# Optimization experiments

Hardware: AMD Instinct MI355X
Metric: run time of the kernel (lower is better)

## Reference

```python
import jax, jax.numpy as jnp
import numpy as np

B, I, H = 256, 512, 512


def _lin_init(k, out_dim, in_dim):
    bound = 1.0 / np.sqrt(in_dim)
    kw, kb = jax.random.split(k)
    W = jax.random.uniform(kw, (out_dim, in_dim), minval=-bound, maxval=bound, dtype=jnp.float32)
    b = jax.random.uniform(kb, (out_dim,), minval=-bound, maxval=bound, dtype=jnp.float32)
    return W, b


def setup_inputs() -> dict:
    key = jax.random.key(0)
    ks = jax.random.split(key, 16)
    inp = {}
    inp['inputs'] = jax.random.normal(ks[0], (B, I), dtype=jnp.float32)
    inp['h0'] = jax.random.normal(ks[1], (B, H), dtype=jnp.float32) * 0.1
    inp['c0'] = jax.random.normal(ks[2], (B, H), dtype=jnp.float32) * 0.1
    inp['hebb'] = jax.random.uniform(ks[3], (B, H, H), minval=-0.01, maxval=0.01, dtype=jnp.float32)
    # plastic recurrent weights: w = 0.02*rand - 0.01, alpha = 1e-4*rand
    inp['w'] = 0.02 * jax.random.uniform(ks[4], (H, H), dtype=jnp.float32) - 0.01
    inp['alpha'] = 1e-4 * jax.random.uniform(ks[5], (1, 1, H), dtype=jnp.float32)
    inp['Wxf'], inp['bxf'] = _lin_init(ks[6], H, I)
    inp['Whf'], inp['bhf'] = _lin_init(ks[7], H, H)
    inp['Wxi'], inp['bxi'] = _lin_init(ks[8], H, I)
    inp['Whi'], inp['bhi'] = _lin_init(ks[9], H, H)
    inp['Wxo'], inp['bxo'] = _lin_init(ks[10], H, I)
    inp['Who'], inp['bho'] = _lin_init(ks[11], H, H)
    inp['Wxc'], inp['bxc'] = _lin_init(ks[12], H, I)
    inp['Wmod'], inp['bmod'] = _lin_init(ks[13], 1, H)   # h2mod: H -> 1
    inp['Wfan'], inp['bfan'] = _lin_init(ks[14], H, 1)   # modfanout: 1 -> H
    return inp


def reference(inputs, h0, c0, hebb, w, alpha,
              Wxf, bxf, Whf, bhf, Wxi, bxi, Whi, bhi,
              Wxo, bxo, Who, bho, Wxc, bxc, Wmod, bmod, Wfan, bfan):
    # gates (torch Linear: y = x @ W.T + b)
    fgt = jax.nn.sigmoid(inputs @ Wxf.T + bxf + h0 @ Whf.T + bhf)
    ipt = jax.nn.sigmoid(inputs @ Wxi.T + bxi + h0 @ Whi.T + bhi)
    opt = jax.nn.sigmoid(inputs @ Wxo.T + bxo + h0 @ Who.T + bho)
    # plastic recurrent path: h0 @ (w + alpha * hebb), per-sample fast weights
    h2c = jnp.einsum('bh,bhk->bk', h0, w + alpha * hebb)
    inputstocell = jnp.tanh(inputs @ Wxc.T + bxc + h2c)
    cell = fgt * c0 + ipt * inputstocell
    hactiv = opt * jnp.tanh(cell)
    # Hebbian outer-product trace update with neuromodulated learning rate
    deltahebb = jnp.einsum('bh,bk->bhk', h0, inputstocell)  # [B,H,H]
    myeta = jnp.tanh(hactiv @ Wmod.T + bmod)                # [B,1]
    myeta = myeta * Wfan[:, 0][None, :] + bfan              # modfanout(1->H): [B,H]
    hebb_new = jnp.clip(hebb + myeta[:, None, :] * deltahebb, -2.0, 2.0)
    return hactiv, cell, hebb_new
```

## Files before the change

### kernel.cpp

```cpp
#include <hip/hip_runtime.h>
#include <math.h>

#define B_ 256
#define I_ 512
#define H_ 512
#define BH (B_*H_)
#define NCH 8
#define HCH (H_/NCH)

typedef float f4v __attribute__((ext_vector_type(4)));


#define TK 16
#define LDT2 34
#define TILE_F (TK*LDT2)
#define NGEMM 512

__global__ __launch_bounds__(256) void k_dot_gates(
    const float* __restrict__ hebb, const float* __restrict__ h0,
    const float* __restrict__ inputs,
    const float* __restrict__ Wxf, const float* __restrict__ bxf,
    const float* __restrict__ Whf, const float* __restrict__ bhf,
    const float* __restrict__ Wxi, const float* __restrict__ bxi,
    const float* __restrict__ Whi, const float* __restrict__ bhi,
    const float* __restrict__ Wxo, const float* __restrict__ bxo,
    const float* __restrict__ Who, const float* __restrict__ bho,
    const float* __restrict__ Wxc, const float* __restrict__ bxc,
    const float* __restrict__ w,
    float* __restrict__ pre, float* __restrict__ part) {

    __shared__ float smem[4 * TILE_F];
    int bid = blockIdx.x;
    int tid = threadIdx.x;

    if (bid < NGEMM) {
        int n0  = (bid >> 3) * 32;
        int m0  = (bid & 7) * 32;
        int g   = n0 >> 9;
        int ko0 = n0 & 511;

        const float* Wx; const float* Wh;
        if (g == 0)      { Wx = Wxf; Wh = Whf; }
        else if (g == 1) { Wx = Wxi; Wh = Whi; }
        else if (g == 2) { Wx = Wxo; Wh = Who; }
        else             { Wx = Wxc; Wh = w;   }

        int tx = tid & 15, ty = tid >> 4;
        int lk = tid & 15, lm = tid >> 4;
        int kk2 = tid >> 4, ln0 = tid & 15;

        float acc[2][2] = {{0.f, 0.f}, {0.f, 0.f}};
        float ar[2], br[2];

        auto LOAD = [&](int t) {
            int k0 = t * TK;
            const float* Ab = (k0 < 512) ? inputs : h0;
            int kbase = k0 & 511;
            #pragma unroll
            for (int p = 0; p < 2; ++p)
                ar[p] = Ab[(size_t)(m0 + lm + 16 * p) * 512 + kbase + lk];
            if (g == 3 && k0 >= 512) {
                #pragma unroll
                for (int p = 0; p < 2; ++p)
                    br[p] = w[(size_t)(kbase + kk2) * 512 + ko0 + ln0 + 16 * p];
            } else {
                const float* Wm = (k0 < 512) ? Wx : Wh;
                #pragma unroll
                for (int p = 0; p < 2; ++p)
                    br[p] = Wm[(size_t)(ko0 + lm + 16 * p) * 512 + kbase + lk];
            }
        };
        auto STORE = [&](int t, int pbuf) {
            float* Asb = smem + pbuf * 2 * TILE_F;
            float* Bsb = Asb + TILE_F;
            int k0 = t * TK;
            #pragma unroll
            for (int p = 0; p < 2; ++p)
                Asb[lk * LDT2 + lm + 16 * p] = ar[p];
            if (g == 3 && k0 >= 512) {
                #pragma unroll
                for (int p = 0; p < 2; ++p)
                    Bsb[kk2 * LDT2 + ln0 + 16 * p] = br[p];
            } else {
                #pragma unroll
                for (int p = 0; p < 2; ++p)
                    Bsb[lk * LDT2 + lm + 16 * p] = br[p];
            }
        };

        LOAD(0);
        STORE(0, 0);
        for (int t = 0; t < 64; ++t) {
            __syncthreads();
            if (t < 63) LOAD(t + 1);
            int pb = t & 1;
            const float* Asb = smem + pb * 2 * TILE_F;
            const float* Bsb = Asb + TILE_F;
            #pragma unroll
            for (int kk = 0; kk < TK; ++kk) {
                float2 a2 = *(const float2*)&Asb[kk * LDT2 + ty * 2];
                float2 b2 = *(const float2*)&Bsb[kk * LDT2 + tx * 2];
                acc[0][0] += a2.x * b2.x; acc[0][1] += a2.x * b2.y;
                acc[1][0] += a2.y * b2.x; acc[1][1] += a2.y * b2.y;
            }
            if (t < 63) STORE(t + 1, pb ^ 1);
        }

        #pragma unroll
        for (int j = 0; j < 2; ++j) {
            int ko = ko0 + tx * 2 + j;
            float bias;
            if (g == 0)      bias = bxf[ko] + bhf[ko];
            else if (g == 1) bias = bxi[ko] + bhi[ko];
            else if (g == 2) bias = bxo[ko] + bho[ko];
            else             bias = bxc[ko];
            #pragma unroll
            for (int i = 0; i < 2; ++i) {
                int bnum = m0 + ty * 2 + i;
                pre[(size_t)g * BH + (size_t)bnum * H_ + ko] = acc[i][j] + bias;
            }
        }
    } else {
        int hbid = bid - NGEMM;
        int b  = hbid >> 3;
        int ch = hbid & 7;

        float*  h0s = smem;
        float4* red = (float4*)(smem + 64);

        if (tid < HCH) h0s[tid] = h0[b * H_ + ch * HCH + tid];
        __syncthreads();

        const float4* hbp = (const float4*)(hebb + ((size_t)b * H_ + (size_t)ch * HCH) * H_);
        int tk = tid & 127;
        int th = tid >> 7;
        float4 acc = make_float4(0.f, 0.f, 0.f, 0.f);
        #pragma unroll 8
        for (int r = 0; r < 32; ++r) {
            int hh = th * 32 + r;
            float s = h0s[hh];
            float4 vv = hbp[(size_t)hh * 128 + tk];
            acc.x += s * vv.x; acc.y += s * vv.y;
            acc.z += s * vv.z; acc.w += s * vv.w;
        }
        red[tid] = acc;
        __syncthreads();
        if (tid < 128) {
            float4 a = red[tid], c = red[tid + 128];
            float4 o = make_float4(a.x + c.x, a.y + c.y, a.z + c.z, a.w + c.w);
            ((float4*)(part + ((size_t)ch * B_ + b) * H_))[tid] = o;
        }
    }
}

__global__ __launch_bounds__(256) void k_finalize(
    const float* __restrict__ pre, const float* __restrict__ part,
    const float* __restrict__ c0, const float* __restrict__ alpha,
    const float* __restrict__ Wmod, const float* __restrict__ bmod,
    const float* __restrict__ Wfan, const float* __restrict__ bfan,
    float* __restrict__ out, float* __restrict__ v) {

    int b = blockIdx.x;
    int t = threadIdx.x;

    float c2r[2];
    float local = 0.f;
    #pragma unroll
    for (int s = 0; s < 2; ++s) {
        int k = t + s * 256;
        float dot = 0.f;
        #pragma unroll
        for (int c = 0; c < NCH; ++c) dot += part[((size_t)c * B_ + b) * H_ + k];
        float pf = pre[0 * BH + (size_t)b * H_ + k];
        float pi = pre[1 * BH + (size_t)b * H_ + k];
        float po = pre[2 * BH + (size_t)b * H_ + k];
        float pc = pre[3 * BH + (size_t)b * H_ + k];
        float c2 = tanhf(pc + alpha[k] * dot);
        float fg = 1.f / (1.f + expf(-pf));
        float ig = 1.f / (1.f + expf(-pi));
        float og = 1.f / (1.f + expf(-po));
        float cell = fg * c0[(size_t)b * H_ + k] + ig * c2;
        float ha = og * tanhf(cell);
        out[(size_t)b * H_ + k] = ha;
        out[BH + (size_t)b * H_ + k] = cell;
        c2r[s] = c2;
        local += ha * Wmod[k];
    }
    float x = local;
    #pragma unroll
    for (int off = 32; off > 0; off >>= 1) x += __shfl_down(x, off, 64);
    __shared__ float red[4];
    int wid = t >> 6, lane = t & 63;
    if (lane == 0) red[wid] = x;
    __syncthreads();
    float s4 = red[0] + red[1] + red[2] + red[3];
    float myeta = tanhf(s4 + bmod[0]);
    #pragma unroll
    for (int s = 0; s < 2; ++s) {
        int k = t + s * 256;
        v[(size_t)b * H_ + k] = (myeta * Wfan[k] + bfan[k]) * c2r[s];
    }
}

__global__ __launch_bounds__(256) void k_update(
    const float4* __restrict__ hebb, const float* __restrict__ h0,
    const float* __restrict__ v, float* __restrict__ out) {
    const int total = B_ * H_ * (H_ / 4);
    int stride = gridDim.x * blockDim.x;
    int base = blockIdx.x * blockDim.x + threadIdx.x;
    for (int f = total - stride + base; f >= 0; f -= stride) {
        int k4 = f & 127;
        int h  = (f >> 7) & 511;
        int b  = f >> 16;
        float u = h0[(b << 9) + h];
        const float4* vv4 = (const float4*)v;
        float4 vv = vv4[(b << 7) + k4];
        float4 hb = hebb[f];
        f4v r;
        r.x = fminf(fmaxf(hb.x + u * vv.x, -2.f), 2.f);
        r.y = fminf(fmaxf(hb.y + u * vv.y, -2.f), 2.f);
        r.z = fminf(fmaxf(hb.z + u * vv.z, -2.f), 2.f);
        r.w = fminf(fmaxf(hb.w + u * vv.w, -2.f), 2.f);
        __builtin_nontemporal_store(r, (f4v*)(out) + f);
    }
}

extern "C" void kernel_launch(void* const* d_in, const int* in_sizes, int n_in,
                              void* d_out, int out_size, void* d_ws, size_t ws_size,
                              hipStream_t stream) {
    const float* inputs = (const float*)d_in[0];
    const float* h0     = (const float*)d_in[1];
    const float* c0     = (const float*)d_in[2];
    const float* hebb   = (const float*)d_in[3];
    const float* w      = (const float*)d_in[4];
    const float* alpha  = (const float*)d_in[5];
    const float* Wxf = (const float*)d_in[6];  const float* bxf = (const float*)d_in[7];
    const float* Whf = (const float*)d_in[8];  const float* bhf = (const float*)d_in[9];
    const float* Wxi = (const float*)d_in[10]; const float* bxi = (const float*)d_in[11];
    const float* Whi = (const float*)d_in[12]; const float* bhi = (const float*)d_in[13];
    const float* Wxo = (const float*)d_in[14]; const float* bxo = (const float*)d_in[15];
    const float* Who = (const float*)d_in[16]; const float* bho = (const float*)d_in[17];
    const float* Wxc = (const float*)d_in[18]; const float* bxc = (const float*)d_in[19];
    const float* Wmod = (const float*)d_in[20]; const float* bmod = (const float*)d_in[21];
    const float* Wfan = (const float*)d_in[22]; const float* bfan = (const float*)d_in[23];

    float* out = (float*)d_out;
    float* ws  = (float*)d_ws;
    float* pre  = ws;
    float* part = ws + 4 * BH;
    float* vbuf = ws + 12 * BH;

    k_dot_gates<<<NGEMM + B_ * NCH, 256, 0, stream>>>(
        hebb, h0, inputs,
        Wxf, bxf, Whf, bhf, Wxi, bxi, Whi, bhi,
        Wxo, bxo, Who, bho, Wxc, bxc, w, pre, part);
    k_finalize<<<B_, 256, 0, stream>>>(pre, part, c0, alpha, Wmod, bmod,
                                       Wfan, bfan, out, vbuf);
    k_update<<<2048, 256, 0, stream>>>((const float4*)hebb, h0, vbuf,
                                       out + 2 * BH);
}
```

Before: 178.5 us.

## Split gate GEMM along K into input and hidden halves, sum in finalize

The gate GEMM now runs as two separate K-halves, inputs@Wx and h0@Wh. Each half writes its own partial pre-activation buffer, and the finalize kernel adds the two halves plus the biases. This doubles the number of GEMM blocks and cuts each block's serial K loop from 64 to 16 iterations. The tile depth is doubled and global loads are widened to float4. The cost is an extra 4*B*H of workspace traffic, and the sums move into finalize.

Result: faster. 171.6 us (-3.9%).

```diff
diff --git a/kernel.cpp b/kernel.cpp
--- a/kernel.cpp
+++ b/kernel.cpp
@@ -11,22 +11,18 @@
 typedef float f4v __attribute__((ext_vector_type(4)));
 
 
-#define TK 16
-#define LDT2 34
-#define TILE_F (TK*LDT2)
-#define NGEMM 512
+#define TK 32
+#define LDB 34
+#define TILE_F (TK*LDB)
+#define NGEMM 1024
 
 __global__ __launch_bounds__(256) void k_dot_gates(
     const float* __restrict__ hebb, const float* __restrict__ h0,
     const float* __restrict__ inputs,
-    const float* __restrict__ Wxf, const float* __restrict__ bxf,
-    const float* __restrict__ Whf, const float* __restrict__ bhf,
-    const float* __restrict__ Wxi, const float* __restrict__ bxi,
-    const float* __restrict__ Whi, const float* __restrict__ bhi,
-    const float* __restrict__ Wxo, const float* __restrict__ bxo,
-    const float* __restrict__ Who, const float* __restrict__ bho,
-    const float* __restrict__ Wxc, const float* __restrict__ bxc,
-    const float* __restrict__ w,
+    const float* __restrict__ Wxf, const float* __restrict__ Whf,
+    const float* __restrict__ Wxi, const float* __restrict__ Whi,
+    const float* __restrict__ Wxo, const float* __restrict__ Who,
+    const float* __restrict__ Wxc, const float* __restrict__ w,
     float* __restrict__ pre, float* __restrict__ part) {
 
     __shared__ float smem[4 * TILE_F];
@@ -34,90 +30,80 @@
     int tid = threadIdx.x;
 
     if (bid < NGEMM) {
-        int n0  = (bid >> 3) * 32;
-        int m0  = (bid & 7) * 32;
-        int g   = n0 >> 9;
+        int ks = bid & 1;
+        int m0 = ((bid >> 1) & 7) * 32;
+        int n0 = (bid >> 4) * 32;
+        int g  = n0 >> 9;
         int ko0 = n0 & 511;
 
-        const float* Wx; const float* Wh;
-        if (g == 0)      { Wx = Wxf; Wh = Whf; }
-        else if (g == 1) { Wx = Wxi; Wh = Whi; }
-        else if (g == 2) { Wx = Wxo; Wh = Who; }
-        else             { Wx = Wxc; Wh = w;   }
-
-        int tx = tid & 15, ty = tid >> 4;
-        int lk = tid & 15, lm = tid >> 4;
-        int kk2 = tid >> 4, ln0 = tid & 15;
+        const float* Asrc = ks ? h0 : inputs;
+        const float* Bsrc;
+        bool wpath = false;
+        if (ks == 0) {
+            Bsrc = (g == 0) ? Wxf : (g == 1) ? Wxi : (g == 2) ? Wxo : Wxc;
+        } else {
+            if (g == 3) { Bsrc = w; wpath = true; }
+            else Bsrc = (g == 0) ? Whf : (g == 1) ? Whi : Who;
+        }
+
+        int row = tid >> 3;
+        int c4  = tid & 7;
+        int tx  = tid & 15, ty = tid >> 4;
 
         float acc[2][2] = {{0.f, 0.f}, {0.f, 0.f}};
-        float ar[2], br[2];
+        float4 areg, breg;
 
         auto LOAD = [&](int t) {
-            int k0 = t * TK;
-            const float* Ab = (k0 < 512) ? inputs : h0;
-            int kbase = k0 & 511;
+            int kb = t * TK;
+            areg = *(const float4*)&Asrc[(size_t)(m0 + row) * 512 + kb + c4 * 4];
+            if (wpath)
+                breg = *(const float4*)&Bsrc[(size_t)(kb + row) * 512 + ko0 + c4 * 4];
+            else
+                breg = *(const float4*)&Bsrc[(size_t)(ko0 + row) * 512 + kb + c4 * 4];
+        };
+        auto STORE = [&](int pbuf) {
+            float* As = smem + pbuf * 2 * TILE_F;
+            float* Bs = As + TILE_F;
             #pragma unroll
-            for (int p = 0; p < 2; ++p)
-                ar[p] = Ab[(size_t)(m0 + lm + 16 * p) * 512 + kbase + lk];
-            if (g == 3 && k0 >= 512) {
+            for (int j = 0; j < 4; ++j)
+                As[(c4 * 4 + j) * LDB + row] = ((const float*)&areg)[j];
+            if (wpath) {
                 #pragma unroll
-                for (int p = 0; p < 2; ++p)
-                    br[p] = w[(size_t)(kbase + kk2) * 512 + ko0 + ln0 + 16 * p];
+                for (int j = 0; j < 4; ++j)
+                    Bs[row * LDB + c4 * 4 + j] = ((const float*)&breg)[j];
             } else {
-                const float* Wm = (k0 < 512) ? Wx : Wh;
                 #pragma unroll
-                for (int p = 0; p < 2; ++p)
-                    br[p] = Wm[(size_t)(ko0 + lm + 16 * p) * 512 + kbase + lk];
+                for (int j = 0; j < 4; ++j)
+                    Bs[(c4 * 4 + j) * LDB + row] = ((const float*)&breg)[j];
             }
         };
-        auto STORE = [&](int t, int pbuf) {
-            float* Asb = smem + pbuf * 2 * TILE_F;
-            float* Bsb = Asb + TILE_F;
-            int k0 = t * TK;
-            #pragma unroll
-            for (int p = 0; p < 2; ++p)
-                Asb[lk * LDT2 + lm + 16 * p] = ar[p];
-            if (g == 3 && k0 >= 512) {
-                #pragma unroll
-                for (int p = 0; p < 2; ++p)
-                    Bsb[kk2 * LDT2 + ln0 + 16 * p] = br[p];
-            } else {
-                #pragma unroll
-                for (int p = 0; p < 2; ++p)
-                    Bsb[lk * LDT2 + lm + 16 * p] = br[p];
-            }
-        };
 
         LOAD(0);
-        STORE(0, 0);
-        for (int t = 0; t < 64; ++t) {
+        STORE(0);
+        for (int t = 0; t < 16; ++t) {
             __syncthreads();
-            if (t < 63) LOAD(t + 1);
+            if (t < 15) LOAD(t + 1);
             int pb = t & 1;
-            const float* Asb = smem + pb * 2 * TILE_F;
-            const float* Bsb = Asb + TILE_F;
+            const float* As = smem + pb * 2 * TILE_F;
+            const float* Bs = As + TILE_F;
             #pragma unroll
             for (int kk = 0; kk < TK; ++kk) {
-                float2 a2 = *(const float2*)&Asb[kk * LDT2 + ty * 2];
-                float2 b2 = *(const float2*)&Bsb[kk * LDT2 + tx * 2];
+                float2 a2 = *(const float2*)&As[kk * LDB + ty * 2];
+                float2 b2 = *(const float2*)&Bs[kk * LDB + tx * 2];
                 acc[0][0] += a2.x * b2.x; acc[0][1] += a2.x * b2.y;
                 acc[1][0] += a2.y * b2.x; acc[1][1] += a2.y * b2.y;
             }
-            if (t < 63) STORE(t + 1, pb ^ 1);
-        }
-
+            if (t < 15) STORE(pb ^ 1);
+        }
+
+        float* pb_out = pre + (size_t)(ks * 4 + g) * BH;
         #pragma unroll
-        for (int j = 0; j < 2; ++j) {
-            int ko = ko0 + tx * 2 + j;
-            float bias;
-            if (g == 0)      bias = bxf[ko] + bhf[ko];
-            else if (g == 1) bias = bxi[ko] + bhi[ko];
-            else if (g == 2) bias = bxo[ko] + bho[ko];
-            else             bias = bxc[ko];
+        for (int i = 0; i < 2; ++i) {
             #pragma unroll
-            for (int i = 0; i < 2; ++i) {
+            for (int j = 0; j < 2; ++j) {
                 int bnum = m0 + ty * 2 + i;
-                pre[(size_t)g * BH + (size_t)bnum * H_ + ko] = acc[i][j] + bias;
+                int ko = ko0 + tx * 2 + j;
+                pb_out[(size_t)bnum * H_ + ko] = acc[i][j];
             }
         }
     } else {
@@ -156,6 +142,10 @@
 __global__ __launch_bounds__(256) void k_finalize(
     const float* __restrict__ pre, const float* __restrict__ part,
     const float* __restrict__ c0, const float* __restrict__ alpha,
+    const float* __restrict__ bxf, const float* __restrict__ bhf,
+    const float* __restrict__ bxi, const float* __restrict__ bhi,
+    const float* __restrict__ bxo, const float* __restrict__ bho,
+    const float* __restrict__ bxc,
     const float* __restrict__ Wmod, const float* __restrict__ bmod,
     const float* __restrict__ Wfan, const float* __restrict__ bfan,
     float* __restrict__ out, float* __restrict__ v) {
@@ -171,18 +161,19 @@
         float dot = 0.f;
         #pragma unroll
         for (int c = 0; c < NCH; ++c) dot += part[((size_t)c * B_ + b) * H_ + k];
-        float pf = pre[0 * BH + (size_t)b * H_ + k];
-        float pi = pre[1 * BH + (size_t)b * H_ + k];
-        float po = pre[2 * BH + (size_t)b * H_ + k];
-        float pc = pre[3 * BH + (size_t)b * H_ + k];
+        size_t off = (size_t)b * H_ + k;
+        float pf = pre[0 * BH + off] + pre[4 * BH + off] + bxf[k] + bhf[k];
+        float pi = pre[1 * BH + off] + pre[5 * BH + off] + bxi[k] + bhi[k];
+        float po = pre[2 * BH + off] + pre[6 * BH + off] + bxo[k] + bho[k];
+        float pc = pre[3 * BH + off] + pre[7 * BH + off] + bxc[k];
         float c2 = tanhf(pc + alpha[k] * dot);
         float fg = 1.f / (1.f + expf(-pf));
         float ig = 1.f / (1.f + expf(-pi));
         float og = 1.f / (1.f + expf(-po));
-        float cell = fg * c0[(size_t)b * H_ + k] + ig * c2;
+        float cell = fg * c0[off] + ig * c2;
         float ha = og * tanhf(cell);
-        out[(size_t)b * H_ + k] = ha;
-        out[BH + (size_t)b * H_ + k] = cell;
+        out[off] = ha;
+        out[BH + off] = cell;
         c2r[s] = c2;
         local += ha * Wmod[k];
     }
@@ -247,15 +238,15 @@
     float* out = (float*)d_out;
     float* ws  = (float*)d_ws;
     float* pre  = ws;
-    float* part = ws + 4 * BH;
-    float* vbuf = ws + 12 * BH;
+    float* part = ws + 8 * BH;
+    float* vbuf = ws + 16 * BH;
 
     k_dot_gates<<<NGEMM + B_ * NCH, 256, 0, stream>>>(
         hebb, h0, inputs,
-        Wxf, bxf, Whf, bhf, Wxi, bxi, Whi, bhi,
-        Wxo, bxo, Who, bho, Wxc, bxc, w, pre, part);
-    k_finalize<<<B_, 256, 0, stream>>>(pre, part, c0, alpha, Wmod, bmod,
-                                       Wfan, bfan, out, vbuf);
+        Wxf, Whf, Wxi, Whi, Wxo, Who, Wxc, w, pre, part);
+    k_finalize<<<B_, 256, 0, stream>>>(pre, part, c0, alpha,
+                                       bxf, bhf, bxi, bhi, bxo, bho, bxc,
+                                       Wmod, bmod, Wfan, bfan, out, vbuf);
     k_update<<<2048, 256, 0, stream>>>((const float4*)hebb, h0, vbuf,
                                        out + 2 * BH);
 }
```
